# Optimization experiments

Hardware: AMD Instinct MI355X
Metric: run time of the kernel (lower is better)

The kernel has to match this reference:

```python
import jax, jax.numpy as jnp
import numpy as np
from itertools import permutations

M = 10          # number of masked tokens (logits.size(0) when whole_word=False)
VOCAB = 50257   # n_class


def setup_inputs() -> dict:
    key = jax.random.key(0)
    k1, k2 = jax.random.split(key)
    logits = jax.random.normal(k1, (M, VOCAB), dtype=jnp.float32)
    target = jax.random.randint(k2, (M,), 0, VOCAB, dtype=jnp.int64).astype(jnp.int32)
    # All M! permutations, enumerated exactly as itertools.permutations (lexicographic),
    # matching the torch module's iteration order (ties broken by first strict improvement).
    perms = jnp.asarray(np.array(list(permutations(range(M))), dtype=np.int32))
    return {"logits": logits, "target": target, "perms": perms}


def reference(logits, target, perms):
    # prob[i, v] = softmax over classes
    prob = jax.nn.softmax(logits, axis=-1)                      # [M, V]
    # S[i, j] = prob[i, target[j]]  (score of assigning slot j's target to position i)
    S = prob[:, target]                                         # [M, M]
    # score(p) = sum_i prob[i, target[p[i]]] = sum_i S[i, p[i]]
    rows = jnp.arange(S.shape[0], dtype=jnp.int32)[None, :]     # [1, M]
    scores = S[rows, perms].sum(axis=-1)                        # [P]
    # torch loop keeps the FIRST permutation achieving the max (strict > update);
    # jnp.argmax also returns the first occurrence of the max.
    best = jnp.argmax(scores)
    target_best = target[perms[best]]                           # [M]
    # CrossEntropyLoss(reduction='none') == -log_softmax gathered at target
    logp = jax.nn.log_softmax(logits, axis=-1)                  # [M, V]
    loss = -jnp.take_along_axis(logp, target_best[:, None].astype(jnp.int32), axis=1)[:, 0]
    return loss, target_best
```

## Files before the change

### kernel.cpp

```cpp
#include <hip/hip_runtime.h>

#define VOCAB 50257
#define M 10
#define NPERM 3628800
#define CHUNKS 16
#define CH 3144
#define NTHREADS_PERM 30240
#define PERM_BLOCKS 60

#define WS_PSUM 0

__global__ __launch_bounds__(256) void chunkstats_kernel(
    const float* __restrict__ logits, float* __restrict__ ws,
    unsigned int* __restrict__ counter, unsigned long long* __restrict__ best) {
    if (blockIdx.x == 0 && threadIdx.x == 0) {
        atomicExch(counter, 0u);
        atomicExch(best, 0ull);
    }
    const int r = blockIdx.x >> 4;
    const int c = blockIdx.x & 15;
    const size_t rowoff = (size_t)r * VOCAB;
    const float* __restrict__ x = logits + rowoff;
    const int s = c * CH;
    const int e = (s + CH < VOCAB) ? s + CH : VOCAB;
    const int tid = threadIdx.x;
    const int j0 = s + (int)((4u - ((unsigned)rowoff & 3u)) & 3u);
    const int j1 = j0 + ((e - j0) & ~3);
    __shared__ float wred[4];

    float sum = 0.f;
    for (int j = s + tid; j < j0; j += 256) sum += expf(x[j]);
    for (int j = j0 + 4 * tid; j < j1; j += 1024) {
        const float4 v = *(const float4*)(x + j);
        sum += expf(v.x) + expf(v.y) + expf(v.z) + expf(v.w);
    }
    for (int j = j1 + tid; j < e; j += 256) sum += expf(x[j]);
    #pragma unroll
    for (int off = 32; off; off >>= 1) sum += __shfl_down(sum, off, 64);
    if ((tid & 63) == 0) wred[tid >> 6] = sum;
    __syncthreads();
    if (tid == 0)
        ws[WS_PSUM + blockIdx.x] = wred[0] + wred[1] + wred[2] + wred[3];
}

__global__ __launch_bounds__(512) void perm_final_kernel(
    const float* __restrict__ logits, const int* __restrict__ target,
    const float* __restrict__ ws, unsigned long long* __restrict__ best,
    unsigned int* __restrict__ counter, float* __restrict__ out) {
    __shared__ float S[100], rowsum[10];
    __shared__ unsigned long long wk[8];
    __shared__ int perm[10];
    __shared__ int lastFlag;
    const int tid = threadIdx.x;

    if (tid < 160) {
        float c = ws[WS_PSUM + tid];
        #pragma unroll
        for (int off = 8; off; off >>= 1) c += __shfl_xor(c, off, 16);
        if ((tid & 15) == 0) rowsum[tid >> 4] = c;
    }
    __syncthreads();
    if (tid < 100) {
        const int i = tid / 10, k = tid % 10;
        S[tid] = expf(logits[(size_t)i * VOCAB + target[k]]) / rowsum[i];
    }
    __syncthreads();

    const unsigned int t = blockIdx.x * 512u + tid;
    unsigned long long key = 0ull;
    if (t < NTHREADS_PERM) {
        const unsigned int base = t * 120u;
        unsigned int p = base;
        unsigned long long avail = 0x9876543210ull;
        float prefix = 0.f;
        const unsigned int fact5[5] = {362880u, 40320u, 5040u, 720u, 120u};
        #pragma unroll
        for (int pos = 0; pos < 5; ++pos) {
            const unsigned int f = fact5[pos];
            const unsigned int d = p / f;
            p -= d * f;
            const unsigned int sh = d * 4u;
            const unsigned int sym = (unsigned int)(avail >> sh) & 0xFu;
            avail = (avail & ((1ull << sh) - 1ull)) | ((avail >> (sh + 4u)) << sh);
            prefix += S[pos * 10 + sym];
        }
        float s5v[5], s6v[5], s7v[5], s8v[5], s9v[5];
        #pragma unroll
        for (int j = 0; j < 5; ++j) {
            const int q = (int)((avail >> (4 * j)) & 0xFull);
            s5v[j] = S[50 + q]; s6v[j] = S[60 + q]; s7v[j] = S[70 + q];
            s8v[j] = S[80 + q]; s9v[j] = S[90 + q];
        }
        float bestsc = -1.f; unsigned int bl = 0; unsigned int l = 0;
        #pragma unroll
        for (int a = 0; a < 5; ++a) {
            const float pa = prefix + s5v[a];
            #pragma unroll
            for (int b = 0; b < 5; ++b) {
                if (b == a) continue;
                const float pb = pa + s6v[b];
                #pragma unroll
                for (int c = 0; c < 5; ++c) {
                    if (c == a || c == b) continue;
                    const float pc = pb + s7v[c];
                    #pragma unroll
                    for (int d = 0; d < 5; ++d) {
                        if (d == a || d == b || d == c) continue;
                        const int e = 10 - a - b - c - d;
                        const float sc = (pc + s8v[d]) + s9v[e];
                        if (sc > bestsc) { bestsc = sc; bl = l; }
                        ++l;
                    }
                }
            }
        }
        const unsigned int gidx = base + bl;
        key = ((unsigned long long)__float_as_uint(bestsc) << 32) |
              (unsigned long long)(0xFFFFFFFFu - gidx);
    }
    #pragma unroll
    for (int off = 32; off; off >>= 1) {
        const unsigned long long o = __shfl_down(key, off, 64);
        if (o > key) key = o;
    }
    if ((tid & 63) == 0) wk[tid >> 6] = key;
    __syncthreads();
    if (tid == 0) {
        unsigned long long k = wk[0];
        #pragma unroll
        for (int w = 1; w < 8; ++w) if (wk[w] > k) k = wk[w];
        atomicMax(best, k);
        __threadfence();
        const unsigned int prev = atomicAdd(counter, 1u);
        lastFlag = (prev == PERM_BLOCKS - 1) ? 1 : 0;
    }
    __syncthreads();
    if (!lastFlag) return;

    if (tid == 0) {
        const unsigned long long kk = atomicAdd(best, 0ull);
        unsigned int p = 0xFFFFFFFFu - (unsigned int)(kk & 0xFFFFFFFFull);
        unsigned long long avail = 0x9876543210ull;
        const unsigned int fact[9] = {362880u, 40320u, 5040u, 720u, 120u, 24u, 6u, 2u, 1u};
        #pragma unroll
        for (int pos = 0; pos < 9; ++pos) {
            const unsigned int f = fact[pos];
            const unsigned int d = p / f;
            p -= d * f;
            const unsigned int sh = d * 4u;
            perm[pos] = (int)((avail >> sh) & 0xFull);
            avail = (avail & ((1ull << sh) - 1ull)) | ((avail >> (sh + 4u)) << sh);
        }
        perm[9] = (int)(avail & 0xFull);
    }
    __syncthreads();
    if (tid < 10) {
        const int tb = target[perm[tid]];
        const float logp = logits[(size_t)tid * VOCAB + tb] - logf(rowsum[tid]);
        out[tid]      = -logp;
        out[10 + tid] = (float)tb;
    }
}

extern "C" void kernel_launch(void* const* d_in, const int* in_sizes, int n_in,
                              void* d_out, int out_size, void* d_ws, size_t ws_size,
                              hipStream_t stream) {
    const float* logits = (const float*)d_in[0];
    const int*   target = (const int*)d_in[1];
    float* ws = (float*)d_ws;
    unsigned int* counter = (unsigned int*)((char*)d_ws + 2048);
    unsigned long long* best = (unsigned long long*)((char*)d_ws + 2056);
    float* out = (float*)d_out;

    chunkstats_kernel<<<10 * CHUNKS, 256, 0, stream>>>(logits, ws, counter, best);
    perm_final_kernel<<<PERM_BLOCKS, 512, 0, stream>>>(logits, target, ws, best,
                                                       counter, out);
}
```

Baseline: 16.32 us.

## Fuse softmax row-sum and permutation search into one kernel with grid barrier

Merges the two kernels into a single 60-block kernel. Each block first computes a chunk of a row's exp-sum, then all blocks meet at a spin-wait grid barrier on a global counter before the permutation search. Counter and best-key reset move to a hipMemsetAsync. This drops the second kernel launch and the gap between kernels, but relies on all 60 blocks being resident at once and adds a memset on the stream.

```diff
diff --git a/kernel.cpp b/kernel.cpp
--- a/kernel.cpp
+++ b/kernel.cpp
@@ -3,61 +3,70 @@
 #define VOCAB 50257
 #define M 10
 #define NPERM 3628800
-#define CHUNKS 16
-#define CH 3144
+#define NBLOCKS 60
+#define CPR 6
+#define CH 8380
 #define NTHREADS_PERM 30240
-#define PERM_BLOCKS 60
 
-#define WS_PSUM 0
 
-__global__ __launch_bounds__(256) void chunkstats_kernel(
-    const float* __restrict__ logits, float* __restrict__ ws,
-    unsigned int* __restrict__ counter, unsigned long long* __restrict__ best) {
-    if (blockIdx.x == 0 && threadIdx.x == 0) {
-        atomicExch(counter, 0u);
-        atomicExch(best, 0ull);
-    }
-    const int r = blockIdx.x >> 4;
-    const int c = blockIdx.x & 15;
+__global__ __launch_bounds__(512) void fused_kernel(
+    const float* __restrict__ logits, const int* __restrict__ target,
+    float* __restrict__ slots, unsigned int* __restrict__ counter,
+    unsigned long long* __restrict__ best, float* __restrict__ out) {
+    __shared__ float wred[8], cv[NBLOCKS], rowsum[10], S[100];
+    __shared__ unsigned long long wk[8];
+    __shared__ int perm[10];
+    __shared__ int lastFlag;
+    const int tid = threadIdx.x;
+    const int bid = blockIdx.x;
+
+    const int r = bid / CPR;
+    const int c = bid - r * CPR;
     const size_t rowoff = (size_t)r * VOCAB;
     const float* __restrict__ x = logits + rowoff;
     const int s = c * CH;
     const int e = (s + CH < VOCAB) ? s + CH : VOCAB;
-    const int tid = threadIdx.x;
     const int j0 = s + (int)((4u - ((unsigned)rowoff & 3u)) & 3u);
     const int j1 = j0 + ((e - j0) & ~3);
-    __shared__ float wred[4];
 
     float sum = 0.f;
-    for (int j = s + tid; j < j0; j += 256) sum += expf(x[j]);
-    for (int j = j0 + 4 * tid; j < j1; j += 1024) {
-        const float4 v = *(const float4*)(x + j);
-        sum += expf(v.x) + expf(v.y) + expf(v.z) + expf(v.w);
+    for (int j = s + tid; j < j0; j += 512) sum += expf(x[j]);
+    #pragma unroll
+    for (int k = 0; k < 5; ++k) {
+        const int j = j0 + 4 * tid + 2048 * k;
+        if (j < j1) {
+            const float4 v = *(const float4*)(x + j);
+            sum += expf(v.x) + expf(v.y) + expf(v.z) + expf(v.w);
+        }
     }
-    for (int j = j1 + tid; j < e; j += 256) sum += expf(x[j]);
+    for (int j = j1 + tid; j < e; j += 512) sum += expf(x[j]);
     #pragma unroll
     for (int off = 32; off; off >>= 1) sum += __shfl_down(sum, off, 64);
     if ((tid & 63) == 0) wred[tid >> 6] = sum;
     __syncthreads();
-    if (tid == 0)
-        ws[WS_PSUM + blockIdx.x] = wred[0] + wred[1] + wred[2] + wred[3];
-}
+    if (tid == 0) {
+        float bsum = wred[0];
+        #pragma unroll
+        for (int w = 1; w < 8; ++w) bsum += wred[w];
+        atomicExch(&slots[bid], bsum);
+        __threadfence();
+        atomicAdd(counter, 1u);
+        while (__hip_atomic_load(counter, __ATOMIC_RELAXED,
+                                 __HIP_MEMORY_SCOPE_AGENT) < NBLOCKS)
+            __builtin_amdgcn_s_sleep(2);
+    }
+    __syncthreads();
+    __threadfence();
 
-__global__ __launch_bounds__(512) void perm_final_kernel(
-    const float* __restrict__ logits, const int* __restrict__ target,
-    const float* __restrict__ ws, unsigned long long* __restrict__ best,
-    unsigned int* __restrict__ counter, float* __restrict__ out) {
-    __shared__ float S[100], rowsum[10];
-    __shared__ unsigned long long wk[8];
-    __shared__ int perm[10];
-    __shared__ int lastFlag;
-    const int tid = threadIdx.x;
-
-    if (tid < 160) {
-        float c = ws[WS_PSUM + tid];
+    if (tid < NBLOCKS)
+        cv[tid] = __hip_atomic_load(&slots[tid], __ATOMIC_RELAXED,
+                                    __HIP_MEMORY_SCOPE_AGENT);
+    __syncthreads();
+    if (tid < 10) {
+        float a = 0.f;
         #pragma unroll
-        for (int off = 8; off; off >>= 1) c += __shfl_xor(c, off, 16);
-        if ((tid & 15) == 0) rowsum[tid >> 4] = c;
+        for (int k = 0; k < CPR; ++k) a += cv[tid * CPR + k];
+        rowsum[tid] = a;
     }
     __syncthreads();
     if (tid < 100) {
@@ -66,7 +75,7 @@
     }
     __syncthreads();
 
-    const unsigned int t = blockIdx.x * 512u + tid;
+    const unsigned int t = bid * 512u + tid;
     unsigned long long key = 0ull;
     if (t < NTHREADS_PERM) {
         const unsigned int base = t * 120u;
@@ -100,14 +109,14 @@
                 if (b == a) continue;
                 const float pb = pa + s6v[b];
                 #pragma unroll
-                for (int c = 0; c < 5; ++c) {
-                    if (c == a || c == b) continue;
-                    const float pc = pb + s7v[c];
+                for (int cc = 0; cc < 5; ++cc) {
+                    if (cc == a || cc == b) continue;
+                    const float pc = pb + s7v[cc];
                     #pragma unroll
                     for (int d = 0; d < 5; ++d) {
-                        if (d == a || d == b || d == c) continue;
-                        const int e = 10 - a - b - c - d;
-                        const float sc = (pc + s8v[d]) + s9v[e];
+                        if (d == a || d == b || d == cc) continue;
+                        const int ee = 10 - a - b - cc - d;
+                        const float sc = (pc + s8v[d]) + s9v[ee];
                         if (sc > bestsc) { bestsc = sc; bl = l; }
                         ++l;
                     }
@@ -132,7 +141,7 @@
         atomicMax(best, k);
         __threadfence();
         const unsigned int prev = atomicAdd(counter, 1u);
-        lastFlag = (prev == PERM_BLOCKS - 1) ? 1 : 0;
+        lastFlag = (prev == 2 * NBLOCKS - 1) ? 1 : 0;
     }
     __syncthreads();
     if (!lastFlag) return;
@@ -167,12 +176,12 @@
                               hipStream_t stream) {
     const float* logits = (const float*)d_in[0];
     const int*   target = (const int*)d_in[1];
-    float* ws = (float*)d_ws;
-    unsigned int* counter = (unsigned int*)((char*)d_ws + 2048);
-    unsigned long long* best = (unsigned long long*)((char*)d_ws + 2056);
+    float* slots = (float*)d_ws;
+    unsigned int* counter = (unsigned int*)((char*)d_ws + 1024);
+    unsigned long long* best = (unsigned long long*)((char*)d_ws + 1032);
     float* out = (float*)d_out;
 
-    chunkstats_kernel<<<10 * CHUNKS, 256, 0, stream>>>(logits, ws, counter, best);
-    perm_final_kernel<<<PERM_BLOCKS, 512, 0, stream>>>(logits, target, ws, best,
-                                                       counter, out);
+    hipMemsetAsync((char*)d_ws + 1024, 0, 16, stream);
+    fused_kernel<<<NBLOCKS, 512, 0, stream>>>(logits, target, slots, counter,
+                                              best, out);
 }
```

Result: slower. 26.96 us (+65.2%).
